# Kernel optimization log

Measured on AMD Instinct MI355X. Metric: run time of the kernel, lower is better.

The kernel has to match this reference:

```python
import jax, jax.numpy as jnp
import numpy as np

DIM = 1024
NHEADS = 16
HEAD_DIM = DIM // NHEADS


def setup_inputs() -> dict:
    key = jax.random.key(0)
    ks = jax.random.split(key, 11)
    B, S = 4, 2048
    scale = 1.0 / np.sqrt(DIM)
    inp = {
        "Q": jax.random.normal(ks[0], (B, S, DIM), jnp.float32),
        "K": jax.random.normal(ks[1], (B, S, DIM), jnp.float32),
        "V": jax.random.normal(ks[2], (B, S, DIM), jnp.float32),
        "Wq": jax.random.normal(ks[3], (DIM, DIM), jnp.float32) * scale,
        "bq": jnp.zeros((DIM,), jnp.float32),
        "Wk": jax.random.normal(ks[4], (DIM, DIM), jnp.float32) * scale,
        "bk": jnp.zeros((DIM,), jnp.float32),
        "Wv": jax.random.normal(ks[5], (DIM, DIM), jnp.float32) * scale,
        "bv": jnp.zeros((DIM,), jnp.float32),
        "Wo": jax.random.normal(ks[6], (DIM, DIM), jnp.float32) * scale,
        "bo": jnp.zeros((DIM,), jnp.float32),
    }
    return inp


def _split_heads(x):
    # [B, S, D] -> [B, H, S, hd]
    B, S, _ = x.shape
    return x.reshape(B, S, NHEADS, HEAD_DIM).transpose(0, 2, 1, 3)


def reference(Q, K, V, Wq, bq, Wk, bk, Wv, bv, Wo, bo):
    q = _split_heads(Q @ Wq + bq)  # [B,H,S,hd]
    k = _split_heads(K @ Wk + bk)
    v = _split_heads(V @ Wv + bv)
    scores = jnp.einsum("bhqd,bhkd->bhqk", q, k) / np.sqrt(HEAD_DIM)
    attn = jax.nn.softmax(scores, axis=-1)  # dropout p=0 -> identity
    out = jnp.einsum("bhqk,bhkd->bhqd", attn, v)  # [B,H,S,hd]
    B, H, S, hd = out.shape
    out = out.transpose(0, 2, 1, 3).reshape(B, S, H * hd)
    return out @ Wo + bo
```

## Files before the change

### kernel.cpp

```cpp
#include <hip/hip_runtime.h>
#include <hip/hip_bf16.h>
#include <math.h>

#define DIM     1024
#define NHEADS  16
#define HD      64
#define BATCH   4
#define SEQ     2048
#define M_TOT   (BATCH * SEQ)
#define QSCALE  0.180336880111f

using short8 = __attribute__((ext_vector_type(8))) short;
using bf16x4 = __attribute__((ext_vector_type(4))) short;
using f32x4  = __attribute__((ext_vector_type(4))) float;

__device__ inline unsigned short f2bf(float x) {
    __hip_bfloat16 h = __float2bfloat16(x);
    unsigned short u;
    __builtin_memcpy(&u, &h, sizeof(u));
    return u;
}
__device__ inline void st_o(float* p, float v)          { *p = v; }
__device__ inline void st_o(unsigned short* p, float v) { *p = f2bf(v); }

__device__ inline void async16(const void* g, void* l) {
    __builtin_amdgcn_global_load_lds(
        (const __attribute__((address_space(1))) void*)g,
        (__attribute__((address_space(3))) void*)l, 16, 0, 0);
}

__global__ __launch_bounds__(256) void cvt3(
    const float* __restrict__ S0, const float* __restrict__ S1,
    const float* __restrict__ S2,
    unsigned short* __restrict__ D0, unsigned short* __restrict__ D1,
    unsigned short* __restrict__ D2)
{
    const float* src; unsigned short* dst;
    switch (blockIdx.y) {
        case 0:  src = S0; dst = D0; break;
        case 1:  src = S1; dst = D1; break;
        default: src = S2; dst = D2; break;
    }
    const size_t i = ((size_t)blockIdx.x * 256 + threadIdx.x) * 16;
    unsigned short tmp[16];
    #pragma unroll
    for (int p = 0; p < 4; ++p) {
        const float4 v = *(const float4*)(src + i + p * 4);
        tmp[p * 4 + 0] = f2bf(v.x); tmp[p * 4 + 1] = f2bf(v.y);
        tmp[p * 4 + 2] = f2bf(v.z); tmp[p * 4 + 3] = f2bf(v.w);
    }
    *(short8*)(dst + i)     = *(short8*)&tmp[0];
    *(short8*)(dst + i + 8) = *(short8*)&tmp[8];
}

__global__ __launch_bounds__(256) void wcvt4(
    const float* __restrict__ W0, const float* __restrict__ W1,
    const float* __restrict__ W2, const float* __restrict__ W3,
    unsigned short* __restrict__ T0, unsigned short* __restrict__ T1,
    unsigned short* __restrict__ T2, unsigned short* __restrict__ T3)
{
    const float* W; unsigned short* Wt;
    switch (blockIdx.z) {
        case 0:  W = W0; Wt = T0; break;
        case 1:  W = W1; Wt = T1; break;
        case 2:  W = W2; Wt = T2; break;
        default: W = W3; Wt = T3; break;
    }
    __shared__ unsigned short tile[32][33];
    const int t = threadIdx.x;
    const int tx = t & 31, ty = t >> 5;
    const int n0 = blockIdx.x * 32, k0 = blockIdx.y * 32;
    #pragma unroll
    for (int i = 0; i < 4; ++i) {
        const int kk = ty + i * 8;
        tile[kk][tx] = f2bf(W[(size_t)(k0 + kk) * DIM + n0 + tx]);
    }
    __syncthreads();
    #pragma unroll
    for (int i = 0; i < 4; ++i) {
        const int nn = ty + i * 8;
        Wt[(size_t)(n0 + nn) * DIM + k0 + tx] = tile[tx][nn];
    }
}

template <typename TY, bool TRANSV>
__device__ __forceinline__ void gemm_body(
    const unsigned short* A, const unsigned short* Wt,
    const float* bias, TY* Y, float scale,
    unsigned short* As, unsigned short* Bs)
{
    const int t = threadIdx.x;
    const int lane = t & 63, wv = t >> 6;
    const int wm = wv >> 1, wn = wv & 1;
    const int l16 = lane & 15, lq = lane >> 4;
    const int m0 = blockIdx.y * 128, n0 = blockIdx.x * 128;
    const int lrow = lane >> 2;
    const int lcol = (lane & 3) * 8;

    f32x4 acc[4][4] = {};

    for (int k0 = 0; k0 < DIM; k0 += 32) {
        #pragma unroll
        for (int c = 0; c < 2; ++c) {
            const int ci  = wv * 2 + c;
            const int row = ci * 16 + lrow;
            async16(A  + (size_t)(m0 + row) * DIM + k0 + lcol, &As[ci * 512]);
            async16(Wt + (size_t)(n0 + row) * DIM + k0 + lcol, &Bs[ci * 512]);
        }
        __syncthreads();

        short8 af[4], bfr[4];
        #pragma unroll
        for (int mi = 0; mi < 4; ++mi)
            af[mi] = *(const short8*)&As[(wm * 64 + mi * 16 + l16) * 32 + lq * 8];
        #pragma unroll
        for (int nj = 0; nj < 4; ++nj)
            bfr[nj] = *(const short8*)&Bs[(wn * 64 + nj * 16 + l16) * 32 + lq * 8];
        #pragma unroll
        for (int mi = 0; mi < 4; ++mi)
            #pragma unroll
            for (int nj = 0; nj < 4; ++nj)
                acc[mi][nj] = __builtin_amdgcn_mfma_f32_16x16x32_bf16(
                    af[mi], bfr[nj], acc[mi][nj], 0, 0, 0);
        __syncthreads();
    }

    #pragma unroll
    for (int mi = 0; mi < 4; ++mi)
        #pragma unroll
        for (int nj = 0; nj < 4; ++nj) {
            const int row = m0 + wm * 64 + mi * 16 + lq * 4;
            const int col = n0 + wn * 64 + nj * 16 + l16;
            const float bb = bias[col];
            if constexpr (TRANSV) {
                unsigned short o[4];
                #pragma unroll
                for (int r = 0; r < 4; ++r)
                    o[r] = f2bf((acc[mi][nj][r] + bb) * scale);
                const int bb_ = row >> 11, ss = row & (SEQ - 1);
                unsigned short* dst = (unsigned short*)Y +
                    ((size_t)(bb_ * NHEADS + (col >> 6)) * HD + (col & 63)) * SEQ + ss;
                *(bf16x4*)dst = *(const bf16x4*)o;
            } else {
                #pragma unroll
                for (int r = 0; r < 4; ++r)
                    st_o(&Y[(size_t)(row + r) * DIM + col],
                         (acc[mi][nj][r] + bb) * scale);
            }
        }
}

template <typename TY, bool TRANSV = false>
__global__ __launch_bounds__(256) void gemm_a16(
    const unsigned short* __restrict__ A, const unsigned short* __restrict__ Wt,
    const float* __restrict__ bias, TY* __restrict__ Y, float scale)
{
    __shared__ unsigned short As[128 * 32];
    __shared__ unsigned short Bs[128 * 32];
    gemm_body<TY, TRANSV>(A, Wt, bias, Y, scale, As, Bs);
}

__global__ __launch_bounds__(256) void gemm_qk(
    const unsigned short* Aq, const unsigned short* Wtq, const float* bq_,
    unsigned short* Yq,
    const unsigned short* Ak, const unsigned short* Wtk, const float* bk_,
    unsigned short* Yk)
{
    __shared__ unsigned short As[128 * 32];
    __shared__ unsigned short Bs[128 * 32];
    const bool k = blockIdx.z != 0;
    gemm_body<unsigned short, false>(k ? Ak : Aq, k ? Wtk : Wtq, k ? bk_ : bq_,
                                     k ? Yk : Yq, k ? 1.0f : QSCALE, As, Bs);
}

__global__ __launch_bounds__(256) void attn_mfma(
    const unsigned short* qbuf, const unsigned short* __restrict__ kbuf,
    const unsigned short* __restrict__ vtb, unsigned short* ctx)
{
    __shared__ unsigned short Kls[2 * 64 * 64];
    __shared__ unsigned short Vls[2 * 64 * 64];
    __shared__ unsigned short Qls[64 * 64];

    const int t = threadIdx.x;
    const int lane = t & 63, wv = t >> 6;
    const int l16 = lane & 15, lq = lane >> 4;
    const int l7 = l16 & 7;
    const int lqh = lq >> 1, lql4 = (lq & 1) * 4;

    const unsigned lin  = (blockIdx.z * gridDim.y + blockIdx.y) * gridDim.x + blockIdx.x;
    const unsigned xcd  = lin & 7, slot = lin >> 3;
    const unsigned bh   = ((slot >> 5) << 3) | xcd;
    const int b = (int)(bh >> 4), h = (int)(bh & 15);
    const int q0 = (int)(slot & 31) * 64;

    const size_t base  = ((size_t)b * SEQ) * DIM + h * HD;
    const size_t vbase = ((size_t)(b * NHEADS + h)) * HD * SEQ;

    const int rl   = lane >> 3;
    const int gcol = ((lane & 7) ^ rl) << 3;

    {
        const int r = t >> 2, c = (t & 3) * 16;
        const int g0 = c >> 3, rx = r & 7;
        const unsigned short* src = qbuf + base + (size_t)(q0 + r) * DIM + c;
        *(short8*)&Qls[r * 64 + ((g0 ^ rx) << 3)]       = *(const short8*)src;
        *(short8*)&Qls[r * 64 + (((g0 + 1) ^ rx) << 3)] = *(const short8*)(src + 8);
    }
    const int qrow = wv * 16 + l16;
    const short8 qf0 = *(const short8*)&Qls[qrow * 64 + ((lq ^ l7) << 3)];
    const short8 qf1 = *(const short8*)&Qls[qrow * 64 + (((4 + lq) ^ l7) << 3)];

    float l_acc = 0.f;
    f32x4 O[4] = {};

    #pragma unroll
    for (int c = 0; c < 2; ++c) {
        const int ci = wv * 2 + c;
        async16(kbuf + base + (size_t)(ci * 8 + rl) * DIM + gcol, Kls + ci * 512);
        async16(vtb + vbase + (size_t)(ci * 8 + rl) * SEQ + gcol, Vls + ci * 512);
    }
    __syncthreads();

    int cur = 0;
    for (int s0 = 0; s0 < SEQ; s0 += 64) {
        const unsigned short* Kc = Kls + cur * 4096;
        const unsigned short* Vc = Vls + cur * 4096;

        if (s0 + 64 < SEQ) {
            unsigned short* Kd = Kls + (cur ^ 1) * 4096;
            unsigned short* Vd = Vls + (cur ^ 1) * 4096;
            #pragma unroll
            for (int c = 0; c < 2; ++c) {
                const int ci = wv * 2 + c;
                async16(kbuf + base + (size_t)(s0 + 64 + ci * 8 + rl) * DIM + gcol,
                        Kd + ci * 512);
                async16(vtb + vbase + (size_t)(ci * 8 + rl) * SEQ + s0 + 64 + gcol,
                        Vd + ci * 512);
            }
        }

        f32x4 sa[4] = {};
        #pragma unroll
        for (int ti = 0; ti < 4; ++ti) {
            const int rr = ti * 16 + l16;
            const short8 kf0 = *(const short8*)(Kc + rr * 64 + ((lq ^ l7) << 3));
            const short8 kf1 = *(const short8*)(Kc + rr * 64 + (((4 + lq) ^ l7) << 3));
            sa[ti] = __builtin_amdgcn_mfma_f32_16x16x32_bf16(kf0, qf0, sa[ti], 0, 0, 0);
            sa[ti] = __builtin_amdgcn_mfma_f32_16x16x32_bf16(kf1, qf1, sa[ti], 0, 0, 0);
        }

        #pragma unroll
        for (int ti = 0; ti < 4; ++ti) {
            const float v0 = __builtin_amdgcn_exp2f(sa[ti][0]);
            const float v1 = __builtin_amdgcn_exp2f(sa[ti][1]);
            const float v2 = __builtin_amdgcn_exp2f(sa[ti][2]);
            const float v3 = __builtin_amdgcn_exp2f(sa[ti][3]);
            l_acc += (v0 + v1) + (v2 + v3);
            bf16x4 pa;
            pa[0] = (short)f2bf(v0); pa[1] = (short)f2bf(v1);
            pa[2] = (short)f2bf(v2); pa[3] = (short)f2bf(v3);
            #pragma unroll
            for (int dt = 0; dt < 4; ++dt) {
                const int vr = dt * 16 + l16;
                const bf16x4 vb = *(const bf16x4*)(
                    Vc + vr * 64 + (((2 * ti + lqh) ^ l7) << 3) + lql4);
                O[dt] = __builtin_amdgcn_mfma_f32_16x16x16bf16_1k(pa, vb, O[dt], 0, 0, 0);
            }
        }

        __syncthreads();
        cur ^= 1;
    }

    l_acc += __shfl_xor(l_acc, 16);
    l_acc += __shfl_xor(l_acc, 32);

    unsigned short (*Ol)[72] = (unsigned short(*)[72])Kls;
    #pragma unroll
    for (int r = 0; r < 4; ++r) {
        const float inv = 1.0f / __shfl(l_acc, lq * 4 + r);
        const int orow = wv * 16 + lq * 4 + r;
        #pragma unroll
        for (int dt = 0; dt < 4; ++dt)
            Ol[orow][dt * 16 + l16] = f2bf(O[dt][r] * inv);
    }
    __syncthreads();
    {
        const int r = t >> 2, c = (t & 3) * 16;
        unsigned short* dst = ctx + base + (size_t)(q0 + r) * DIM + c;
        *(short8*)dst       = *(const short8*)&Ol[r][c];
        *(short8*)(dst + 8) = *(const short8*)&Ol[r][c + 8];
    }
}

extern "C" void kernel_launch(void* const* d_in, const int* in_sizes, int n_in,
                              void* d_out, int out_size, void* d_ws, size_t ws_size,
                              hipStream_t stream) {
    const float* Q  = (const float*)d_in[0];
    const float* K  = (const float*)d_in[1];
    const float* V  = (const float*)d_in[2];
    const float* Wq = (const float*)d_in[3];
    const float* bq = (const float*)d_in[4];
    const float* Wk = (const float*)d_in[5];
    const float* bk = (const float*)d_in[6];
    const float* Wv = (const float*)d_in[7];
    const float* bv = (const float*)d_in[8];
    const float* Wo = (const float*)d_in[9];
    const float* bo = (const float*)d_in[10];
    float* out = (float*)d_out;

    const size_t eW = (size_t)DIM * DIM;
    const size_t eB = (size_t)M_TOT * DIM;
    unsigned short* p   = (unsigned short*)d_ws;
    unsigned short* wtq = p; p += eW;
    unsigned short* wtk = p; p += eW;
    unsigned short* wtv = p; p += eW;
    unsigned short* wto = p; p += eW;
    unsigned short* bufA = p; p += eB;
    unsigned short* bufB = p; p += eB;
    unsigned short* bufC = p; p += eB;
    unsigned short* bufD = p; p += eB;
    unsigned short* bufE = p;

    wcvt4<<<dim3(32, 32, 4), 256, 0, stream>>>(Wq, Wk, Wv, Wo, wtq, wtk, wtv, wto);

    const int cvt_blocks = (int)(eB / (256 * 16));
    cvt3<<<dim3(cvt_blocks, 3), 256, 0, stream>>>(V, Q, K, bufA, bufC, bufB);

    const dim3 gg(DIM / 128, M_TOT / 128);

    gemm_a16<unsigned short, true><<<gg, 256, 0, stream>>>(
        bufA, wtv, bv, bufE, 1.0f);
    gemm_qk<<<dim3(DIM / 128, M_TOT / 128, 2), 256, 0, stream>>>(
        bufC, wtq, bq, bufA,
        bufB, wtk, bk, bufD);

    attn_mfma<<<dim3(SEQ / 64, NHEADS, BATCH), 256, 0, stream>>>(bufA, bufD, bufE, bufA);

    gemm_a16<float><<<gg, 256, 0, stream>>>(bufA, wto, bo, out, 1.0f);
}
```

Before: 384.7 us.

## Double-buffer GEMM shared-memory tiles and reuse K buffer for Q staging in attention

The projection GEMM mainloop now prefetches the next K-slice of A and W into a second shared-memory buffer while MFMAs run on the current one. This aims to hide global-to-LDS load latency behind compute, and it drops one of the two barriers per iteration. The attention kernel stops using a separate Q shared buffer and stages Q through the K buffer instead, with a barrier added after the Q fragments are read into registers. This cuts LDS use, which may allow more blocks per CU. The cost is double the GEMM LDS footprint and one extra barrier at the start of attention.

```diff
diff --git a/kernel.cpp b/kernel.cpp
--- a/kernel.cpp
+++ b/kernel.cpp
@@ -99,30 +99,47 @@
 
     f32x4 acc[4][4] = {};
 
+    #pragma unroll
+    for (int c = 0; c < 2; ++c) {
+        const int ci  = wv * 2 + c;
+        const int row = ci * 16 + lrow;
+        async16(A  + (size_t)(m0 + row) * DIM + lcol, &As[ci * 512]);
+        async16(Wt + (size_t)(n0 + row) * DIM + lcol, &Bs[ci * 512]);
+    }
+    __syncthreads();
+
+    int cur = 0;
     for (int k0 = 0; k0 < DIM; k0 += 32) {
-        #pragma unroll
-        for (int c = 0; c < 2; ++c) {
-            const int ci  = wv * 2 + c;
-            const int row = ci * 16 + lrow;
-            async16(A  + (size_t)(m0 + row) * DIM + k0 + lcol, &As[ci * 512]);
-            async16(Wt + (size_t)(n0 + row) * DIM + k0 + lcol, &Bs[ci * 512]);
-        }
-        __syncthreads();
+        if (k0 + 32 < DIM) {
+            unsigned short* Ad = As + (cur ^ 1) * 4096;
+            unsigned short* Bd = Bs + (cur ^ 1) * 4096;
+            #pragma unroll
+            for (int c = 0; c < 2; ++c) {
+                const int ci  = wv * 2 + c;
+                const int row = ci * 16 + lrow;
+                async16(A  + (size_t)(m0 + row) * DIM + k0 + 32 + lcol, Ad + ci * 512);
+                async16(Wt + (size_t)(n0 + row) * DIM + k0 + 32 + lcol, Bd + ci * 512);
+            }
+        }
+        const unsigned short* Ac = As + cur * 4096;
+        const unsigned short* Bc = Bs + cur * 4096;
 
         short8 af[4], bfr[4];
         #pragma unroll
         for (int mi = 0; mi < 4; ++mi)
-            af[mi] = *(const short8*)&As[(wm * 64 + mi * 16 + l16) * 32 + lq * 8];
+            af[mi] = *(const short8*)&Ac[(wm * 64 + mi * 16 + l16) * 32 + lq * 8];
         #pragma unroll
         for (int nj = 0; nj < 4; ++nj)
-            bfr[nj] = *(const short8*)&Bs[(wn * 64 + nj * 16 + l16) * 32 + lq * 8];
+            bfr[nj] = *(const short8*)&Bc[(wn * 64 + nj * 16 + l16) * 32 + lq * 8];
         #pragma unroll
         for (int mi = 0; mi < 4; ++mi)
             #pragma unroll
             for (int nj = 0; nj < 4; ++nj)
                 acc[mi][nj] = __builtin_amdgcn_mfma_f32_16x16x32_bf16(
                     af[mi], bfr[nj], acc[mi][nj], 0, 0, 0);
+
         __syncthreads();
+        cur ^= 1;
     }
 
     #pragma unroll
@@ -155,8 +172,8 @@
     const unsigned short* __restrict__ A, const unsigned short* __restrict__ Wt,
     const float* __restrict__ bias, TY* __restrict__ Y, float scale)
 {
-    __shared__ unsigned short As[128 * 32];
-    __shared__ unsigned short Bs[128 * 32];
+    __shared__ unsigned short As[2 * 128 * 32];
+    __shared__ unsigned short Bs[2 * 128 * 32];
     gemm_body<TY, TRANSV>(A, Wt, bias, Y, scale, As, Bs);
 }
 
@@ -166,8 +183,8 @@
     const unsigned short* Ak, const unsigned short* Wtk, const float* bk_,
     unsigned short* Yk)
 {
-    __shared__ unsigned short As[128 * 32];
-    __shared__ unsigned short Bs[128 * 32];
+    __shared__ unsigned short As[2 * 128 * 32];
+    __shared__ unsigned short Bs[2 * 128 * 32];
     const bool k = blockIdx.z != 0;
     gemm_body<unsigned short, false>(k ? Ak : Aq, k ? Wtk : Wtq, k ? bk_ : bq_,
                                      k ? Yk : Yq, k ? 1.0f : QSCALE, As, Bs);
@@ -179,7 +196,6 @@
 {
     __shared__ unsigned short Kls[2 * 64 * 64];
     __shared__ unsigned short Vls[2 * 64 * 64];
-    __shared__ unsigned short Qls[64 * 64];
 
     const int t = threadIdx.x;
     const int lane = t & 63, wv = t >> 6;
@@ -203,12 +219,14 @@
         const int r = t >> 2, c = (t & 3) * 16;
         const int g0 = c >> 3, rx = r & 7;
         const unsigned short* src = qbuf + base + (size_t)(q0 + r) * DIM + c;
-        *(short8*)&Qls[r * 64 + ((g0 ^ rx) << 3)]       = *(const short8*)src;
-        *(short8*)&Qls[r * 64 + (((g0 + 1) ^ rx) << 3)] = *(const short8*)(src + 8);
+        *(short8*)&Kls[r * 64 + ((g0 ^ rx) << 3)]       = *(const short8*)src;
+        *(short8*)&Kls[r * 64 + (((g0 + 1) ^ rx) << 3)] = *(const short8*)(src + 8);
     }
     const int qrow = wv * 16 + l16;
-    const short8 qf0 = *(const short8*)&Qls[qrow * 64 + ((lq ^ l7) << 3)];
-    const short8 qf1 = *(const short8*)&Qls[qrow * 64 + (((4 + lq) ^ l7) << 3)];
+    const short8 qf0 = *(const short8*)&Kls[qrow * 64 + ((lq ^ l7) << 3)];
+    const short8 qf1 = *(const short8*)&Kls[qrow * 64 + (((4 + lq) ^ l7) << 3)];
+    asm volatile("" :: "v"(qf0), "v"(qf1));
+    __syncthreads();
 
     float l_acc = 0.f;
     f32x4 O[4] = {};
```

Result: no change. 383.8 us (-0.2%).
